# Optimization experiments

Measured on AMD Instinct MI355X. Metric: run time of the kernel, lower is better.

## Reference

```python
import jax, jax.numpy as jnp
import numpy as np

B, T, V, WD = 32, 2048, 50000, 300        # batch, max_doc_len, batch vocab, word_dim
P, L, ND = 150, 7, 2                      # total patterns, max_pattern_length, num_diags
BIAS_SCALE = 1.0
ZERO = -100.0                             # max-plus semiring zero (repo: neg_infinity = -100*ones)
# end state per pattern = pattern_length - 1, for pattern_specs {5:50, 6:50, 7:50}
END_STATES = np.concatenate([np.full(50, 4), np.full(50, 5), np.full(50, 6)]).astype(np.int32)


def setup_inputs() -> dict:
    key = jax.random.key(0)
    ks = jax.random.split(key, 10)
    diags = jax.random.normal(ks[0], (P * ND * L, WD), jnp.float32)
    diags = diags / jnp.linalg.norm(diags, axis=1, keepdims=True)  # normalize() in __init__
    return {
        "embeddings_matrix": jax.random.normal(ks[1], (WD, V), jnp.float32),
        "diags": diags,
        "bias": jax.random.normal(ks[2], (P * ND * L, 1), jnp.float32),
        "epsilon": jax.random.normal(ks[3], (P, L - 1), jnp.float32),
        "mlp_w0": jax.random.normal(ks[4], (P, 100), jnp.float32) * 0.1,
        "mlp_b0": jnp.zeros((100,), jnp.float32),
        "mlp_w1": jax.random.normal(ks[5], (100, 2), jnp.float32) * 0.1,
        "mlp_b1": jnp.zeros((2,), jnp.float32),
        "docs": jax.random.randint(ks[6], (B, T), 0, V),
        "doc_lens": jax.random.randint(ks[7], (B,), 5, T + 1),
    }


def reference(embeddings_matrix, diags, bias, epsilon, mlp_w0, mlp_b0, mlp_w1, mlp_b1, docs, doc_lens):
    # Max-plus semiring: from_float = identity, times = +, plus = max, one = 0, zero = -100.
    # Transition scores for every token in the batch vocabulary: [V, P*ND*L]
    trans = (diags @ embeddings_matrix + BIAS_SCALE * bias).T
    # Gather per doc token, reshape, time-major: [T, B, P, ND, L]
    tm = trans[docs].reshape(B, T, P, ND, L).transpose(1, 0, 2, 3, 4)

    end_states = jnp.asarray(END_STATES)               # [P]
    active = jnp.arange(T)[:, None] < doc_lens[None, :]  # [T, B]

    zero_pad = jnp.full((B, P, 1), ZERO, trans.dtype)
    restart_pad = jnp.zeros((B, P, 1), trans.dtype)      # semiring one
    hid0 = jnp.full((B, P, L), ZERO, trans.dtype).at[:, :, 0].set(0.0)
    scores0 = jnp.full((B, P), ZERO, trans.dtype)
    eps_val = epsilon                                    # epsilon_scale = semiring one (=0) -> identity

    def step(carry, xs):
        hid, sc = carry
        tmat, act = xs  # tmat: [B, P, ND, L], act: [B]
        # epsilon transitions (shift by one state, additive in max-plus)
        after_eps = jnp.maximum(hid, jnp.concatenate([zero_pad, hid[:, :, :-1] + eps_val], axis=2))
        # main-path transitions (diag index -1), with restart padding at state 0
        main = jnp.concatenate([restart_pad, after_eps[:, :, :-1] + tmat[:, :, -1, :-1]], axis=2)
        # self loops (diag index 0); self_loop_scale = semiring one = 0
        self_loop = hid + tmat[:, :, 0, :]
        hid = jnp.maximum(main, self_loop)
        end_vals = jnp.take_along_axis(hid, end_states[None, :, None], axis=2)[:, :, 0]  # [B, P]
        sc = jnp.where(act[:, None], jnp.maximum(sc, end_vals), sc)
        return (hid, sc), None

    (_, scores), _ = jax.lax.scan(step, (hid0, scores0), (tm, active))
    # MLP head: Linear -> relu -> Linear
    h = scores @ mlp_w0 + mlp_b0
    return jax.nn.relu(h) @ mlp_w1 + mlp_b1
```

## Files before the change

### kernel.cpp

```cpp
#include <hip/hip_runtime.h>
#include <stdint.h>

#define B_   32
#define T_   2048
#define V_   50000
#define WD_  300
#define P_   150
#define KP   320
#define MP   2112
#define MB2  2176
#define NPAD2 50176
#define VT_  391
#define MT_  17
#define NWG3 6664
#define NEGC (-1.0e30f)

#define WS_DIAGSB      32112640u
#define WS_TRANS_BIG   54067200u
#define WS_TRANS_SMALL 33505280u
#define WS_AUX_BIG     265267200u
#define WS_AUX_SMALL   244705280u
#define AUX_BYTES      864260u
#define WS_NEED_BIG    (WS_AUX_BIG + AUX_BYTES)
#define WS_NEED_SMALL  (WS_AUX_SMALL + AUX_BYTES)

typedef __attribute__((ext_vector_type(8))) short bf16x8;
typedef __attribute__((ext_vector_type(4))) float f32x4;

#define GLOAD_LDS16(gp, lp) __builtin_amdgcn_global_load_lds( \
    (__attribute__((address_space(1))) void*)(gp), \
    (__attribute__((address_space(3))) void*)(lp), 16, 0, 0)

__device__ __forceinline__ unsigned short f2bf(float f){
  unsigned u = __builtin_bit_cast(unsigned, f);
  u = u + 0x7fffu + ((u >> 16) & 1u);
  return (unsigned short)(u >> 16);
}
__device__ __forceinline__ float bf_lo(unsigned u){ return __builtin_bit_cast(float, u << 16); }
__device__ __forceinline__ float bf_hi(unsigned u){ return __builtin_bit_cast(float, u & 0xffff0000u); }

__global__ __launch_bounds__(256) void k_transpose_emb(const float* __restrict__ emb,
                                                       unsigned short* __restrict__ embT){
  __shared__ float tile[32][65];
  int v0 = blockIdx.x * 64, k0 = blockIdx.y * 32;
  int tid = threadIdx.x;
  #pragma unroll
  for (int it = 0; it < 8; ++it){
    int idx = it * 256 + tid;
    int kk = idx >> 6, vv = idx & 63;
    int k = k0 + kk, v = v0 + vv;
    float val = 0.f;
    if (k < WD_ && v < V_) val = emb[(size_t)k * V_ + v];
    tile[kk][vv] = val;
  }
  __syncthreads();
  int row = tid >> 2, c = tid & 3;
  unsigned short e[8];
  #pragma unroll
  for (int i = 0; i < 8; ++i) e[i] = f2bf(tile[c*8 + i][row]);
  uint4 pk;
  pk.x = (unsigned)e[0] | ((unsigned)e[1] << 16);
  pk.y = (unsigned)e[2] | ((unsigned)e[3] << 16);
  pk.z = (unsigned)e[4] | ((unsigned)e[5] << 16);
  pk.w = (unsigned)e[6] | ((unsigned)e[7] << 16);
  *(uint4*)&embT[(size_t)(v0 + row) * KP + k0 + c*8] = pk;
}

__global__ __launch_bounds__(256) void k_conv_diags(const float* __restrict__ diags,
                                                    unsigned short* __restrict__ diagsB){
  int gid = blockIdx.x * 256 + threadIdx.x;
  int m = gid / 80;
  int k4 = (gid % 80) * 4;
  unsigned short e[4];
  #pragma unroll
  for (int i = 0; i < 4; ++i){
    int k = k4 + i;
    float v = (m < 2100 && k < WD_) ? diags[m * WD_ + k] : 0.f;
    e[i] = f2bf(v);
  }
  uint2 pk;
  pk.x = (unsigned)e[0] | ((unsigned)e[1] << 16);
  pk.y = (unsigned)e[2] | ((unsigned)e[3] << 16);
  *(uint2*)&diagsB[(size_t)m * KP + k4] = pk;
}

__global__ __launch_bounds__(256) void k_zero(int* __restrict__ used, int* __restrict__ counter){
  int i = blockIdx.x * 256 + threadIdx.x;
  if (i < NPAD2) used[i] = 0;
  if (i == 0) *counter = 0;
}
__global__ __launch_bounds__(256) void k_mark(const int* __restrict__ docs,
                                              const int* __restrict__ dlens,
                                              int* __restrict__ used){
  int i = blockIdx.x * 256 + threadIdx.x;
  int b = i >> 11, t = i & 2047;
  if (t < dlens[b]) used[docs[i]] = 1;
}
__global__ __launch_bounds__(256) void k_compact(const int* __restrict__ used,
                                                 int* __restrict__ remap,
                                                 int* __restrict__ inv,
                                                 int* __restrict__ counter){
  int v = blockIdx.x * 256 + threadIdx.x;
  if (v >= V_) return;
  if (used[v]){
    int id = atomicAdd(counter, 1);
    remap[v] = id;
    inv[id] = v;
  }
}
__global__ __launch_bounds__(256) void k_docsC(const int* __restrict__ docs,
                                               const int* __restrict__ dlens,
                                               const int* __restrict__ remap,
                                               int* __restrict__ docsC){
  int i = blockIdx.x * 256 + threadIdx.x;
  int b = i >> 11, t = i & 2047;
  docsC[i] = (t < dlens[b]) ? remap[docs[i]] : 0;
}

__global__ __launch_bounds__(256, 4) void k_gemm(const unsigned short* __restrict__ embT,
                                                 const unsigned short* __restrict__ diagsB,
                                                 const float* __restrict__ bias,
                                                 const int* __restrict__ inv,
                                                 const int* __restrict__ nusedp,
                                                 unsigned short* __restrict__ trans){
  __shared__ char smem[33792];
  int nused = *nusedp;
  int orig = blockIdx.x;
  int xcd = orig & 7, idx0 = orig >> 3;
  int vt = (idx0 / MT_) * 8 + xcd;
  int mt = idx0 % MT_;
  int v0 = vt * 128, m0 = mt * 128;
  if (v0 >= nused) return;

  int tid = threadIdx.x;
  int w = tid >> 6, l = tid & 63;
  int wv = w & 1, wm = w >> 1;
  int lrow = l & 15, lq = l >> 4;

  int rA0 = tid >> 2, rA1 = 64 + (tid >> 2);
  size_t ga0 = (size_t)((v0 + rA0 < nused) ? inv[v0 + rA0] : 0) * KP;
  size_t ga1 = (size_t)((v0 + rA1 < nused) ? inv[v0 + rA1] : 0) * KP;

  f32x4 acc[4][4];
  #pragma unroll
  for (int i = 0; i < 4; ++i)
    #pragma unroll
    for (int j = 0; j < 4; ++j)
      acc[i][j] = (f32x4){0.f, 0.f, 0.f, 0.f};

  auto STAGE = [&](int buf, int kt){
    int k0 = kt * 32;
    char* bA = smem + buf * 16384;
    char* bB = bA + 8192;
    int slot = tid & 3;
    {
      int idx = tid;
      int sc = slot ^ ((rA0 >> 1) & 3);
      GLOAD_LDS16(&embT[ga0 + k0 + sc * 8], bA + idx * 16);
      int row = idx >> 2;
      int scB = slot ^ ((row >> 1) & 3);
      GLOAD_LDS16(&diagsB[(size_t)(m0 + row) * KP + k0 + scB * 8], bB + idx * 16);
    }
    {
      int idx = 256 + tid;
      int sc = slot ^ ((rA1 >> 1) & 3);
      GLOAD_LDS16(&embT[ga1 + k0 + sc * 8], bA + idx * 16);
      int row = idx >> 2;
      int scB = slot ^ ((row >> 1) & 3);
      GLOAD_LDS16(&diagsB[(size_t)(m0 + row) * KP + k0 + scB * 8], bB + idx * 16);
    }
  };

  STAGE(0, 0);
  #pragma unroll
  for (int kt = 0; kt < 10; ++kt){
    if (kt < 9){
      STAGE((kt + 1) & 1, kt + 1);
      asm volatile("s_waitcnt vmcnt(4)" ::: "memory");
    } else {
      asm volatile("s_waitcnt vmcnt(0)" ::: "memory");
    }
    __builtin_amdgcn_s_barrier();
    __builtin_amdgcn_sched_barrier(0);
    char* bA = smem + (kt & 1) * 16384;
    char* bB = bA + 8192;
    bf16x8 af[4], bg[4];
    #pragma unroll
    for (int i = 0; i < 4; ++i){
      int row = wv * 64 + i * 16 + lrow;
      af[i] = *(const bf16x8*)(bA + row * 64 + (lq ^ ((row >> 1) & 3)) * 16);
    }
    #pragma unroll
    for (int j = 0; j < 4; ++j){
      int row = wm * 64 + j * 16 + lrow;
      bg[j] = *(const bf16x8*)(bB + row * 64 + (lq ^ ((row >> 1) & 3)) * 16);
    }
    #pragma unroll
    for (int i = 0; i < 4; ++i)
      #pragma unroll
      for (int j = 0; j < 4; ++j)
        acc[i][j] = __builtin_amdgcn_mfma_f32_16x16x32_bf16(af[i], bg[j], acc[i][j], 0, 0, 0);
    __builtin_amdgcn_sched_barrier(0);
    __builtin_amdgcn_s_barrier();
  }

  float bv4[4];
  #pragma unroll
  for (int j = 0; j < 4; ++j){
    int mg = m0 + wm * 64 + j * 16 + lrow;
    bv4[j] = (mg < 2100) ? bias[mg] : 0.f;
  }
  unsigned short* eb = (unsigned short*)smem;
  #pragma unroll
  for (int i = 0; i < 4; ++i)
    #pragma unroll
    for (int j = 0; j < 4; ++j)
      #pragma unroll
      for (int r = 0; r < 4; ++r){
        int row = wv * 64 + i * 16 + lq * 4 + r;
        int col = wm * 64 + j * 16 + lrow;
        eb[row * 132 + col] = f2bf(acc[i][j][r] + bv4[j]);
      }
  __syncthreads();
  #pragma unroll
  for (int it = 0; it < 16; ++it){
    int idx2 = it * 256 + tid;
    int row = idx2 >> 5, chq = idx2 & 31;
    int vg = v0 + row, mg = m0 + chq * 4;
    if (vg < nused && mg < MP){
      uint2 val = *(const uint2*)(smem + row * 264 + chq * 8);
      *(uint2*)&trans[(size_t)vg * MP + mg] = val;
    }
  }
}

template<int CH>
__global__ __launch_bounds__(192) void k_scan(const unsigned short* __restrict__ trans,
                                              const int* __restrict__ docsC,
                                              const int* __restrict__ doc_lens,
                                              const float* __restrict__ epsilon,
                                              float* __restrict__ chunkout){
  constexpr int NCHT = T_ / CH;
  constexpr int NG = CH / 4;
  __shared__ int sdocs[CH];
  __shared__ char rows[2][4][4224];
  int b = blockIdx.x / NCHT, ch = blockIdx.x % NCHT;
  int doclen = doc_lens[b];
  int tbase = ch * CH;
  if (tbase >= doclen) return;
  int tid = threadIdx.x;
  if (tid < CH) sdocs[tid] = docsC[b * T_ + tbase + tid];
  __syncthreads();
  int p = tid;
  bool act_p = p < P_;
  float eps_r[6] = {0,0,0,0,0,0};
  int endsel = 0;
  if (act_p){
    #pragma unroll
    for (int i = 0; i < 6; ++i) eps_r[i] = epsilon[p*6 + i];
    endsel = p / 50;
  }

  float col[7][7], bvec[7], uvec[7], w;
  #pragma unroll
  for (int j = 0; j < 7; ++j)
    #pragma unroll
    for (int l = 0; l < 7; ++l) col[j][l] = (j == l) ? 0.f : NEGC;
  #pragma unroll
  for (int l = 0; l < 7; ++l){ bvec[l] = NEGC; uvec[l] = NEGC; }
  w = NEGC;

  const char* transB = (const char*)trans;

  uint4 rg[4][2];
  #pragma unroll
  for (int r = 0; r < 4; ++r){ rg[r][0] = make_uint4(0,0,0,0); rg[r][1] = make_uint4(0,0,0,0); }

  auto LOADG = [&](int g){
    #pragma unroll
    for (int r = 0; r < 4; ++r){
      const uint4* src = (const uint4*)(transB + (size_t)sdocs[g*4 + r] * (MP*2));
      rg[r][0] = src[tid];
      if (tid < 72) rg[r][1] = src[192 + tid];
    }
  };
  auto WRITEG = [&](int buf){
    #pragma unroll
    for (int r = 0; r < 4; ++r){
      uint4* dst = (uint4*)rows[buf][r];
      dst[tid] = rg[r][0];
      if (tid < 72) dst[192 + tid] = rg[r][1];
    }
  };

  auto stepL = [&](const char* rp, bool act){
    unsigned q[7];
    #pragma unroll
    for (int i = 0; i < 7; ++i) q[i] = *(const unsigned*)(rp + 4*i);
    float tsf[7], tmn[6];
    tsf[0]=bf_lo(q[0]); tsf[1]=bf_hi(q[0]);
    tsf[2]=bf_lo(q[1]); tsf[3]=bf_hi(q[1]);
    tsf[4]=bf_lo(q[2]); tsf[5]=bf_hi(q[2]);
    tsf[6]=bf_lo(q[3]); tmn[0]=bf_hi(q[3]);
    tmn[1]=bf_lo(q[4]); tmn[2]=bf_hi(q[4]);
    tmn[3]=bf_lo(q[5]); tmn[4]=bf_hi(q[5]);
    tmn[5]=bf_lo(q[6]);
    #pragma unroll
    for (int j = 0; j < 7; ++j){
      #pragma unroll
      for (int l = 6; l >= 1; --l){
        if (l < j) continue;
        if (l == j){ col[j][l] = col[j][l] + tsf[l]; continue; }
        float ae;
        if (l - 1 == j) ae = col[j][l-1];
        else ae = fmaxf(col[j][l-1], col[j][l-2] + eps_r[l-2]);
        col[j][l] = fmaxf(ae + tmn[l-1], col[j][l] + tsf[l]);
      }
      if (j == 0) col[0][0] += tsf[0];
    }
    #pragma unroll
    for (int l = 6; l >= 1; --l){
      float ae;
      if (l == 1) ae = fmaxf(bvec[0], -100.0f);
      else ae = fmaxf(bvec[l-1], bvec[l-2] + eps_r[l-2]);
      bvec[l] = fmaxf(ae + tmn[l-1], bvec[l] + tsf[l]);
    }
    bvec[0] = fmaxf(0.0f, bvec[0] + tsf[0]);
    if (act){
      #pragma unroll
      for (int j = 0; j < 7; ++j){
        float c4 = (j <= 4) ? col[j][4] : NEGC;
        float c5 = (j <= 5) ? col[j][5] : NEGC;
        float c6 = col[j][6];
        float ce = (endsel == 0) ? c4 : ((endsel == 1) ? c5 : c6);
        uvec[j] = fmaxf(uvec[j], ce);
      }
      float be = (endsel == 0) ? bvec[4] : ((endsel == 1) ? bvec[5] : bvec[6]);
      w = fmaxf(w, be);
    }
  };

  LOADG(0); WRITEG(0); __syncthreads();
  for (int g = 0; g < NG; ++g){
    if (g + 1 < NG) LOADG(g + 1);
    if (act_p){
      #pragma unroll
      for (int r = 0; r < 4; ++r)
        stepL(&rows[g & 1][r][p * 28], (tbase + g*4 + r) < doclen);
    }
    __syncthreads();
    if (g + 1 < NG) WRITEG((g + 1) & 1);
    __syncthreads();
  }

  if (act_p){
    float out[44];
    int idx = 0;
    #pragma unroll
    for (int j = 0; j < 7; ++j)
      #pragma unroll
      for (int l = j; l < 7; ++l) out[idx++] = col[j][l];
    #pragma unroll
    for (int l = 0; l < 7; ++l) out[28 + l] = bvec[l];
    #pragma unroll
    for (int l = 0; l < 7; ++l) out[35 + l] = uvec[l];
    out[42] = w; out[43] = 0.f;
    float* dst = chunkout + ((size_t)(b * NCHT + ch) * P_ + p) * 44;
    #pragma unroll
    for (int i = 0; i < 11; ++i){
      float4 t2 = make_float4(out[4*i], out[4*i+1], out[4*i+2], out[4*i+3]);
      ((float4*)dst)[i] = t2;
    }
  }
}

__global__ __launch_bounds__(192) void k_combine_mlp(const float* __restrict__ chunkout,
                                                     const int* __restrict__ doc_lens,
                                                     const float* __restrict__ w0,
                                                     const float* __restrict__ b0,
                                                     const float* __restrict__ w1,
                                                     const float* __restrict__ b1,
                                                     float* __restrict__ out,
                                                     int nch, int chsz){
  __shared__ float ssc[P_];
  __shared__ float sh[100];
  int b = blockIdx.x, tid = threadIdx.x;
  if (tid < P_){
    int p = tid;
    int doclen = doc_lens[b];
    int nact = (doclen + chsz - 1) / chsz;
    if (nact > nch) nact = nch;
    float h[7] = {0.f, -100.f, -100.f, -100.f, -100.f, -100.f, -100.f};
    float sc = -100.f;
    for (int ch = 0; ch < nact; ++ch){
      const float* rec = chunkout + ((size_t)(b * nch + ch) * P_ + p) * 44;
      float r[44];
      #pragma unroll
      for (int i = 0; i < 11; ++i){
        float4 t = ((const float4*)rec)[i];
        r[4*i] = t.x; r[4*i+1] = t.y; r[4*i+2] = t.z; r[4*i+3] = t.w;
      }
      #pragma unroll
      for (int j = 0; j < 7; ++j) sc = fmaxf(sc, r[35 + j] + h[j]);
      sc = fmaxf(sc, r[42]);
      constexpr int off[7] = {0, 7, 13, 18, 22, 25, 27};
      float nh[7];
      #pragma unroll
      for (int l = 0; l < 7; ++l){
        float v = r[28 + l];
        #pragma unroll
        for (int j = 0; j < 7; ++j){
          if (j <= l) v = fmaxf(v, r[off[j] + (l - j)] + h[j]);
        }
        nh[l] = v;
      }
      #pragma unroll
      for (int l = 0; l < 7; ++l) h[l] = nh[l];
    }
    ssc[p] = sc;
  }
  __syncthreads();
  if (tid < 100){
    float a = b0[tid];
    for (int pp = 0; pp < P_; ++pp) a += ssc[pp] * w0[pp * 100 + tid];
    sh[tid] = fmaxf(a, 0.f);
  }
  __syncthreads();
  if (tid < 2){
    float o = b1[tid];
    for (int j = 0; j < 100; ++j) o += sh[j] * w1[j * 2 + tid];
    out[b * 2 + tid] = o;
  }
}

extern "C" void kernel_launch(void* const* d_in, const int* in_sizes, int n_in,
                              void* d_out, int out_size, void* d_ws, size_t ws_size,
                              hipStream_t stream){
  const float* emb   = (const float*)d_in[0];
  const float* diags = (const float*)d_in[1];
  const float* bias  = (const float*)d_in[2];
  const float* eps   = (const float*)d_in[3];
  const float* w0    = (const float*)d_in[4];
  const float* b0    = (const float*)d_in[5];
  const float* w1    = (const float*)d_in[6];
  const float* b1    = (const float*)d_in[7];
  const int* docs    = (const int*)d_in[8];
  const int* dlens   = (const int*)d_in[9];

  if (ws_size < (size_t)WS_NEED_SMALL) return;
  bool big = ws_size >= (size_t)WS_NEED_BIG;

  char* ws = (char*)d_ws;
  unsigned short* embT   = (unsigned short*)(ws);
  unsigned short* diagsB = (unsigned short*)(ws + WS_DIAGSB);
  unsigned short* trans  = (unsigned short*)(ws + (big ? WS_TRANS_BIG : WS_TRANS_SMALL));
  char* aux              = ws + (big ? WS_AUX_BIG : WS_AUX_SMALL);
  int* used    = (int*)(aux);
  int* remap   = (int*)(aux + 200704u);
  int* inv     = (int*)(aux + 401408u);
  int* docsC   = (int*)(aux + 602112u);
  int* counter = (int*)(aux + 864256u);
  float* chunkout = (float*)(ws);
  float* outp = (float*)d_out;

  k_transpose_emb<<<dim3(NPAD2/64, KP/32), 256, 0, stream>>>(emb, embT);
  k_conv_diags<<<(MB2*80 + 255)/256, 256, 0, stream>>>(diags, diagsB);
  k_zero<<<NPAD2/256, 256, 0, stream>>>(used, counter);
  k_mark<<<B_*T_/256, 256, 0, stream>>>(docs, dlens, used);
  k_compact<<<(V_ + 255)/256, 256, 0, stream>>>(used, remap, inv, counter);
  k_docsC<<<B_*T_/256, 256, 0, stream>>>(docs, dlens, remap, docsC);
  k_gemm<<<NWG3, 256, 0, stream>>>(embT, diagsB, bias, inv, counter, trans);
  if (big){
    k_scan<32><<<B_ * 64, 192, 0, stream>>>(trans, docsC, dlens, eps, chunkout);
    k_combine_mlp<<<B_, 192, 0, stream>>>(chunkout, dlens, w0, b0, w1, b1, outp, 64, 32);
  } else {
    k_scan<64><<<B_ * 32, 192, 0, stream>>>(trans, docsC, dlens, eps, chunkout);
    k_combine_mlp<<<B_, 192, 0, stream>>>(chunkout, dlens, w0, b0, w1, b1, outp, 32, 64);
  }
}
```

Before: 199.8 us.

## Give each wavefront its own trans slice so the scan needs no block barriers

Each 64-lane wavefront now loads and stages only the 64 patterns' worth of trans data it consumes (a 1792-byte slice per row) into its own shared-memory region. Because no thread reads another wavefront's data, both __syncthreads calls in the time loop are removed. The group size also drops from 4 tokens to 2 per stage. This cuts per-step barrier and synchronisation cost but halves the prefetch depth, which may expose global-load latency. It also relies on implicit intra-wavefront ordering between the shared-memory writes and reads.

```diff
diff --git a/kernel.cpp b/kernel.cpp
--- a/kernel.cpp
+++ b/kernel.cpp
@@ -241,9 +241,9 @@
                                               const float* __restrict__ epsilon,
                                               float* __restrict__ chunkout){
   constexpr int NCHT = T_ / CH;
-  constexpr int NG = CH / 4;
+  constexpr int NG = CH / 2;
   __shared__ int sdocs[CH];
-  __shared__ char rows[2][4][4224];
+  __shared__ char rows[2][2][3][1792];
   int b = blockIdx.x / NCHT, ch = blockIdx.x % NCHT;
   int doclen = doc_lens[b];
   int tbase = ch * CH;
@@ -251,6 +251,8 @@
   int tid = threadIdx.x;
   if (tid < CH) sdocs[tid] = docsC[b * T_ + tbase + tid];
   __syncthreads();
+
+  int w = tid >> 6, l = tid & 63;
   int p = tid;
   bool act_p = p < P_;
   float eps_r[6] = {0,0,0,0,0,0};
@@ -261,35 +263,38 @@
     endsel = p / 50;
   }
 
-  float col[7][7], bvec[7], uvec[7], w;
+  float col[7][7], bvec[7], uvec[7], wmax;
   #pragma unroll
   for (int j = 0; j < 7; ++j)
     #pragma unroll
-    for (int l = 0; l < 7; ++l) col[j][l] = (j == l) ? 0.f : NEGC;
-  #pragma unroll
-  for (int l = 0; l < 7; ++l){ bvec[l] = NEGC; uvec[l] = NEGC; }
-  w = NEGC;
+    for (int l2 = 0; l2 < 7; ++l2) col[j][l2] = (j == l2) ? 0.f : NEGC;
+  #pragma unroll
+  for (int l2 = 0; l2 < 7; ++l2){ bvec[l2] = NEGC; uvec[l2] = NEGC; }
+  wmax = NEGC;
 
   const char* transB = (const char*)trans;
-
-  uint4 rg[4][2];
-  #pragma unroll
-  for (int r = 0; r < 4; ++r){ rg[r][0] = make_uint4(0,0,0,0); rg[r][1] = make_uint4(0,0,0,0); }
+  int sliceOff = 1792 * w;
+  bool part0 = (w < 2) ? true : (l < 40);
+  bool part1 = (w < 2) && (l < 48);
+
+  uint4 rg[2][2];
+  #pragma unroll
+  for (int r = 0; r < 2; ++r){ rg[r][0] = make_uint4(0,0,0,0); rg[r][1] = make_uint4(0,0,0,0); }
 
   auto LOADG = [&](int g){
     #pragma unroll
-    for (int r = 0; r < 4; ++r){
-      const uint4* src = (const uint4*)(transB + (size_t)sdocs[g*4 + r] * (MP*2));
-      rg[r][0] = src[tid];
-      if (tid < 72) rg[r][1] = src[192 + tid];
+    for (int r = 0; r < 2; ++r){
+      const char* src = transB + (size_t)sdocs[g*2 + r] * (MP*2) + sliceOff;
+      if (part0) rg[r][0] = *(const uint4*)(src + l * 16);
+      if (part1) rg[r][1] = *(const uint4*)(src + (64 + l) * 16);
     }
   };
   auto WRITEG = [&](int buf){
     #pragma unroll
-    for (int r = 0; r < 4; ++r){
-      uint4* dst = (uint4*)rows[buf][r];
-      dst[tid] = rg[r][0];
-      if (tid < 72) dst[192 + tid] = rg[r][1];
+    for (int r = 0; r < 2; ++r){
+      char* dst = rows[buf][r][w];
+      if (part0) *(uint4*)(dst + l * 16) = rg[r][0];
+      if (part1) *(uint4*)(dst + (64 + l) * 16) = rg[r][1];
     }
   };
 
@@ -308,22 +313,22 @@
     #pragma unroll
     for (int j = 0; j < 7; ++j){
       #pragma unroll
-      for (int l = 6; l >= 1; --l){
-        if (l < j) continue;
-        if (l == j){ col[j][l] = col[j][l] + tsf[l]; continue; }
+      for (int l2 = 6; l2 >= 1; --l2){
+        if (l2 < j) continue;
+        if (l2 == j){ col[j][l2] = col[j][l2] + tsf[l2]; continue; }
         float ae;
-        if (l - 1 == j) ae = col[j][l-1];
-        else ae = fmaxf(col[j][l-1], col[j][l-2] + eps_r[l-2]);
-        col[j][l] = fmaxf(ae + tmn[l-1], col[j][l] + tsf[l]);
+        if (l2 - 1 == j) ae = col[j][l2-1];
+        else ae = fmaxf(col[j][l2-1], col[j][l2-2] + eps_r[l2-2]);
+        col[j][l2] = fmaxf(ae + tmn[l2-1], col[j][l2] + tsf[l2]);
       }
       if (j == 0) col[0][0] += tsf[0];
     }
     #pragma unroll
-    for (int l = 6; l >= 1; --l){
+    for (int l2 = 6; l2 >= 1; --l2){
       float ae;
-      if (l == 1) ae = fmaxf(bvec[0], -100.0f);
-      else ae = fmaxf(bvec[l-1], bvec[l-2] + eps_r[l-2]);
-      bvec[l] = fmaxf(ae + tmn[l-1], bvec[l] + tsf[l]);
+      if (l2 == 1) ae = fmaxf(bvec[0], -100.0f);
+      else ae = fmaxf(bvec[l2-1], bvec[l2-2] + eps_r[l2-2]);
+      bvec[l2] = fmaxf(ae + tmn[l2-1], bvec[l2] + tsf[l2]);
     }
     bvec[0] = fmaxf(0.0f, bvec[0] + tsf[0]);
     if (act){
@@ -336,21 +341,19 @@
         uvec[j] = fmaxf(uvec[j], ce);
       }
       float be = (endsel == 0) ? bvec[4] : ((endsel == 1) ? bvec[5] : bvec[6]);
-      w = fmaxf(w, be);
+      wmax = fmaxf(wmax, be);
     }
   };
 
-  LOADG(0); WRITEG(0); __syncthreads();
+  LOADG(0);
+  WRITEG(0);
   for (int g = 0; g < NG; ++g){
     if (g + 1 < NG) LOADG(g + 1);
     if (act_p){
-      #pragma unroll
-      for (int r = 0; r < 4; ++r)
-        stepL(&rows[g & 1][r][p * 28], (tbase + g*4 + r) < doclen);
-    }
-    __syncthreads();
+      stepL(&rows[g & 1][0][w][l * 28], (tbase + g*2)     < doclen);
+      stepL(&rows[g & 1][1][w][l * 28], (tbase + g*2 + 1) < doclen);
+    }
     if (g + 1 < NG) WRITEG((g + 1) & 1);
-    __syncthreads();
   }
 
   if (act_p){
@@ -359,12 +362,12 @@
     #pragma unroll
     for (int j = 0; j < 7; ++j)
       #pragma unroll
-      for (int l = j; l < 7; ++l) out[idx++] = col[j][l];
-    #pragma unroll
-    for (int l = 0; l < 7; ++l) out[28 + l] = bvec[l];
-    #pragma unroll
-    for (int l = 0; l < 7; ++l) out[35 + l] = uvec[l];
-    out[42] = w; out[43] = 0.f;
+      for (int l2 = j; l2 < 7; ++l2) out[idx++] = col[j][l2];
+    #pragma unroll
+    for (int l2 = 0; l2 < 7; ++l2) out[28 + l2] = bvec[l2];
+    #pragma unroll
+    for (int l2 = 0; l2 < 7; ++l2) out[35 + l2] = uvec[l2];
+    out[42] = wmax; out[43] = 0.f;
     float* dst = chunkout + ((size_t)(b * NCHT + ch) * P_ + p) * 44;
     #pragma unroll
     for (int i = 0; i < 11; ++i){
```

Result: faster. 188.6 us (-5.6%).
